# Kernel tuning notes

Measured on AMD Instinct MI355X. Metric: run time of the kernel, lower is better.

Reference implementation:

```python
import jax, jax.numpy as jnp
import numpy as np

B, K, V, D, T = 8, 4, 32000, 1024, 16
EOS, PAD = 2, 0
EOS_SCORE = 1000.0
BIG = 1e9  # suppresses beams 1..K-1 at step 0 (original starts from a single beam)


def setup_inputs() -> dict:
    key = jax.random.key(0)
    k1, k2, k3, k4 = jax.random.split(key, 4)
    s = 1.0 / np.sqrt(D)
    return {
        "words": jnp.ones((B, K), dtype=jnp.int32),  # BOS=1 on every beam
        "h0": jnp.zeros((B, K, D), dtype=jnp.float32),
        "c0": jnp.zeros((B, K, D), dtype=jnp.float32),
        "E": jax.random.normal(k1, (V, D), dtype=jnp.float32) * s,
        "Wx": jax.random.normal(k2, (D, 4 * D), dtype=jnp.float32) * s,
        "Wh": jax.random.normal(k3, (D, 4 * D), dtype=jnp.float32) * s,
        "b": jnp.zeros((4 * D,), dtype=jnp.float32),
        "Wout": jax.random.normal(k4, (D, V), dtype=jnp.float32) * s,
        "bout": jnp.zeros((V,), dtype=jnp.float32),
    }


def reference(words, h0, c0, E, Wx, Wh, b, Wout, bout):
    bidx = jnp.arange(B)[:, None]
    kidx = jnp.arange(K)[None, :]
    scores0 = jnp.concatenate(
        [jnp.zeros((B, 1), jnp.float32), jnp.full((B, K - 1), BIG, jnp.float32)], axis=1)
    buf0 = jnp.zeros((B, K, T), dtype=jnp.int32)
    stopped0 = jnp.zeros((B,), dtype=bool)

    def step(carry, j):
        w, scores, h, c, stopped, buf = carry
        # proc_word: embed -> LSTM cell -> vocab logits (vectorized over B*K beams)
        x = E[w]                                              # [B,K,D]
        gates = jnp.einsum('bkd,df->bkf', x, Wx) + jnp.einsum('bkd,df->bkf', h, Wh) + b
        i_, f_, g_, o_ = jnp.split(gates, 4, axis=-1)
        c_new = jax.nn.sigmoid(f_) * c + jax.nn.sigmoid(i_) * jnp.tanh(g_)
        h_new = jax.nn.sigmoid(o_) * jnp.tanh(c_new)
        logits = jnp.einsum('bkd,dv->bkv', h_new, Wout) + bout  # [B,K,V]
        p = -jax.nn.log_softmax(logits, axis=-1)                # negative log-probs
        neg_ps, idxs = jax.lax.top_k(-p, K)                     # K smallest per beam
        cand = (-neg_ps) + scores[:, :, None]                   # [B,K,K]
        flat = cand.reshape(B, K * K)
        wflat = idxs.reshape(B, K * K)
        neg_sel, sel = jax.lax.top_k(-flat, K)                  # K smallest over all cands
        sel_scores = -neg_sel                                   # [B,K]
        prev = sel // K                                         # originating beam
        new_w = jnp.take_along_axis(wflat, sel, axis=1)
        eos = new_w == EOS
        first_eos = eos[:, 0] & (~stopped)                      # best cand is EOS -> stop
        pen = eos & (~first_eos[:, None]) & (~stopped[:, None]) # non-best EOS penalized
        sel_scores = jnp.where(pen, EOS_SCORE, sel_scores)
        tok = jnp.where(first_eos[:, None], EOS, new_w)
        tok = jnp.where(stopped[:, None], PAD, tok)
        prevb = jnp.where(stopped[:, None], kidx, prev)         # stopped rows keep order
        buf = buf[bidx, prevb]                                  # reorder beam histories
        buf = buf.at[:, :, j].set(tok.astype(jnp.int32))
        h_new = h_new[bidx, prev]                               # gather per-beam states
        c_new = c_new[bidx, prev]
        scores = jnp.where(stopped[:, None], scores, sel_scores)
        w = jnp.where(stopped[:, None], w, new_w.astype(w.dtype))
        stopped = stopped | first_eos
        return (w, scores, h_new, c_new, stopped, buf), None

    carry0 = (words, scores0, h0, c0, stopped0, buf0)
    (_, scores, _, _, _, buf), _ = jax.lax.scan(step, carry0, jnp.arange(T))
    return buf, scores
```

## Files before the change

### kernel.cpp

```cpp
#include <hip/hip_runtime.h>
#include <math.h>
#include <float.h>

namespace {

constexpr int Bb = 8, Kk = 4, BKn = 32, Dd = 1024, Ff = 4096, Vv = 32000, Tt = 16;
constexpr int GDS = 32, GDC = 32;
constexpr int LTW = 64;
constexpr int LNB = Vv / LTW;
constexpr int LQC = 16;
constexpr int LQN = 16;
constexpr int NVCH = LNB;
constexpr int EOSt = 2, PADt = 0;
constexpr float BIGf = 1e9f, EOSSf = 1000.0f;

constexpr size_t OFF_HTN = 0;
constexpr size_t OFF_CB0 = OFF_HTN + (size_t)Dd * BKn;
constexpr size_t OFF_CB1 = OFF_CB0 + (size_t)BKn * Dd;
constexpr size_t OFF_GP  = OFF_CB1 + (size_t)BKn * Dd;
constexpr size_t OFF_CS  = OFF_GP  + (size_t)GDS * BKn * Ff;
constexpr size_t OFF_SC  = OFF_CS  + (size_t)NVCH * BKn * 12;
constexpr size_t OFF_INT = OFF_SC  + BKn;
constexpr int IW = 0, ISTOP = 32, IPREV = 40, IBUFA = 72, IBUFB = IBUFA + Bb * Kk * Tt;

__device__ __forceinline__ void cp16(const float* g, float* l) {
  __builtin_amdgcn_global_load_lds(
      (const __attribute__((address_space(1))) void*)g,
      (__attribute__((address_space(3))) void*)l, 16, 0, 0);
}

__device__ inline void ins4(float v, int id, float tv[4], int ti[4]) {
#pragma unroll
  for (int r = 0; r < 4; r++) {
    bool better = (v > tv[r]) || (v == tv[r] && id < ti[r]);
    if (better) { float fv = tv[r]; int fi = ti[r]; tv[r] = v; ti[r] = id; v = fv; id = fi; }
  }
}

template <int STARTOFF>
__device__ inline void merge_top4(float tv[4], int ti[4], float ov[4], int oi[4]) {
#pragma unroll
  for (int r = 0; r < 4; r++) {
    float hv = tv[0]; int hi = ti[0];
    float m = hv;
    for (int off = STARTOFF; off; off >>= 1) m = fmaxf(m, __shfl_xor(m, off));
    int c = (hv == m) ? hi : 0x7fffffff;
    for (int off = STARTOFF; off; off >>= 1) c = min(c, __shfl_xor(c, off));
    if (hv == m && hi == c) {
      tv[0] = tv[1]; ti[0] = ti[1];
      tv[1] = tv[2]; ti[1] = ti[2];
      tv[2] = tv[3]; ti[2] = ti[3];
      tv[3] = -FLT_MAX; ti[3] = 0x7fffffff;
    }
    ov[r] = m; oi[r] = c;
  }
}

__global__ __launch_bounds__(256) void initK(const int* __restrict__ words,
    const float* __restrict__ h0, const float* __restrict__ c0,
    float* __restrict__ ws) {
  int* wsi = (int*)(ws + OFF_INT);
  if (blockIdx.x < 128) {
    int g = blockIdx.x * 256 + threadIdx.x;
    int d = g >> 5, bk = g & 31;
    ws[OFF_HTN + g] = h0[(size_t)bk * Dd + d];
    ws[OFF_CB0 + g] = c0[g];
  } else {
    int t = threadIdx.x;
    if (t < BKn) {
      ws[OFF_SC + t] = ((t & 3) == 0) ? 0.f : BIGf;
      wsi[IW + t] = words[t];
      wsi[IPREV + t] = t & 3;
    }
    if (t < Bb) wsi[ISTOP + t] = 0;
    for (int i = t; i < 2 * Bb * Kk * Tt; i += 256) wsi[IBUFA + i] = 0;
  }
}

__global__ __launch_bounds__(256) void gatesK(const float* __restrict__ Wx,
    const float* __restrict__ Wh, const float* __restrict__ E,
    const float* __restrict__ hTn, const int* __restrict__ wsi,
    float* __restrict__ Gp) {
  __shared__ float xs[GDC][BKn], hs[GDC][BKn];
  int tid = threadIdx.x;
  int d0 = blockIdx.y * GDC;
  {
    int bk = tid & 31, dq = tid >> 5;
    int w = wsi[IW + bk];
    int src = (bk & ~3) | wsi[IPREV + bk];
    const float* Erow = E + (size_t)w * Dd + d0;
#pragma unroll
    for (int k = 0; k < 4; k++) {
      int d = dq * 4 + k;
      xs[d][bk] = Erow[d];
      hs[d][bk] = hTn[(size_t)(d0 + d) * BKn + src];
    }
  }
  __syncthreads();
  int ct = tid & 31, bg = tid >> 5;
  int f0 = blockIdx.x * 128 + ct * 4;
  float acc[4][4];
#pragma unroll
  for (int c = 0; c < 4; c++)
#pragma unroll
    for (int i = 0; i < 4; i++) acc[c][i] = 0.f;
#pragma unroll 4
  for (int d = 0; d < GDC; ++d) {
    float4 wx = *(const float4*)(Wx + (size_t)(d0 + d) * Ff + f0);
    float4 wh = *(const float4*)(Wh + (size_t)(d0 + d) * Ff + f0);
    float4 x4 = *(const float4*)&xs[d][bg * 4];
    float4 h4 = *(const float4*)&hs[d][bg * 4];
    float xv[4] = {x4.x, x4.y, x4.z, x4.w};
    float hv[4] = {h4.x, h4.y, h4.z, h4.w};
    float wxc[4] = {wx.x, wx.y, wx.z, wx.w};
    float whc[4] = {wh.x, wh.y, wh.z, wh.w};
#pragma unroll
    for (int c = 0; c < 4; c++)
#pragma unroll
      for (int i = 0; i < 4; i++)
        acc[c][i] = fmaf(xv[i], wxc[c], fmaf(hv[i], whc[c], acc[c][i]));
  }
#pragma unroll
  for (int i = 0; i < 4; i++) {
    int bk = bg * 4 + i;
    float4 o = {acc[0][i], acc[1][i], acc[2][i], acc[3][i]};
    *(float4*)(Gp + ((size_t)blockIdx.y * BKn + bk) * Ff + f0) = o;
  }
}

__global__ __launch_bounds__(256) void lstmK(const float* __restrict__ bvec,
    const float* __restrict__ Gp, const float* __restrict__ cPrev,
    const int* __restrict__ wsi, float* __restrict__ cNew,
    float* __restrict__ hTn) {
  __shared__ float part[4][128];
  int bk = blockIdx.x;
  int dcl = threadIdx.x & 127;
  int half = threadIdx.x >> 7;
  int dc = blockIdx.y * 128 + dcl;
  float s[4] = {0.f, 0.f, 0.f, 0.f};
#pragma unroll 4
  for (int dsl = 0; dsl < 16; dsl++) {
    int ds = half * 16 + dsl;
    const float* row = Gp + ((size_t)ds * BKn + bk) * Ff;
#pragma unroll
    for (int g = 0; g < 4; g++) s[g] += row[(size_t)g * Dd + dc];
  }
  if (half == 1) {
#pragma unroll
    for (int g = 0; g < 4; g++) part[g][dcl] = s[g];
  }
  __syncthreads();
  if (half == 0) {
    float gi = s[0] + part[0][dcl] + bvec[dc];
    float gf = s[1] + part[1][dcl] + bvec[Dd + dc];
    float gg = s[2] + part[2][dcl] + bvec[2 * Dd + dc];
    float go = s[3] + part[3][dcl] + bvec[3 * Dd + dc];
    int src = (bk & ~3) | wsi[IPREV + bk];
    float c = cPrev[(size_t)src * Dd + dc];
    float si = 1.f / (1.f + expf(-gi));
    float sf = 1.f / (1.f + expf(-gf));
    float so = 1.f / (1.f + expf(-go));
    float tg = tanhf(gg);
    float cn = sf * c + si * tg;
    float hn = so * tanhf(cn);
    cNew[(size_t)bk * Dd + dc] = cn;
    hTn[(size_t)dc * BKn + bk] = hn;
  }
}

__global__ __launch_bounds__(256) void logitsAK(const float* __restrict__ Wo,
    const float* __restrict__ bo, const float* __restrict__ hTn,
    float* __restrict__ cs) {
  __shared__ float wb[4][3][LQC][LTW];
  __shared__ float hb[4][3][LQC][BKn];
  __shared__ float sd[BKn][LTW];
  int tid = threadIdx.x;
  int q = tid >> 6;
  int lane = tid & 63;
  int cg = lane & 15;
  int bg = lane >> 4;
  size_t v0 = (size_t)blockIdx.x * LTW;
  int dq0 = q * 256;
  float acc[4][8];
#pragma unroll
  for (int c = 0; c < 4; c++)
#pragma unroll
    for (int i = 0; i < 8; i++) acc[c][i] = 0.f;

  float4 b4 = *(const float4*)(bo + v0 + cg * 4);

#define STAGE(CH, B)                                                          \
  {                                                                           \
    int d0_ = dq0 + (CH) * LQC;                                               \
    _Pragma("unroll") for (int i_ = 0; i_ < 4; i_++)                          \
      cp16(Wo + (size_t)(d0_ + i_ * 4 + (lane >> 4)) * Vv + v0 +              \
               (lane & 15) * 4,                                               \
           &wb[q][B][i_ * 4][0]);                                             \
    _Pragma("unroll") for (int j_ = 0; j_ < 2; j_++)                          \
      cp16(hTn + (size_t)(d0_ + j_ * 8 + (lane >> 3)) * BKn + (lane & 7) * 4, \
           &hb[q][B][j_ * 8][0]);                                             \
  }

  STAGE(0, 0)
  STAGE(1, 1)
  for (int k = 0; k < LQN; k++) {
    int b = k % 3;
    if (k + 2 < LQN) {
      STAGE(k + 2, (k + 2) % 3)
      asm volatile("s_waitcnt vmcnt(12)" ::: "memory");
    } else if (k + 1 < LQN) {
      asm volatile("s_waitcnt vmcnt(6)" ::: "memory");
    } else {
      asm volatile("s_waitcnt vmcnt(0)" ::: "memory");
    }
    __builtin_amdgcn_sched_barrier(0);
#pragma unroll 4
    for (int d = 0; d < LQC; d++) {
      float4 w4  = *(const float4*)&wb[q][b][d][cg * 4];
      float4 hlo = *(const float4*)&hb[q][b][d][bg * 8];
      float4 hhi = *(const float4*)&hb[q][b][d][bg * 8 + 4];
      float wv[4] = {w4.x, w4.y, w4.z, w4.w};
      float hv[8] = {hlo.x, hlo.y, hlo.z, hlo.w, hhi.x, hhi.y, hhi.z, hhi.w};
#pragma unroll
      for (int c = 0; c < 4; c++)
#pragma unroll
        for (int i = 0; i < 8; i++)
          acc[c][i] = fmaf(wv[c], hv[i], acc[c][i]);
    }
  }
#undef STAGE

  float bb[4] = {b4.x, b4.y, b4.z, b4.w};
  if (q == 0) {
#pragma unroll
    for (int c = 0; c < 4; c++)
#pragma unroll
      for (int i = 0; i < 8; i++)
        sd[bg * 8 + i][cg * 4 + c] = acc[c][i] + bb[c];
  }
  __syncthreads();
#pragma unroll
  for (int qq = 1; qq < 4; qq++) {
    if (q == qq) {
#pragma unroll
      for (int c = 0; c < 4; c++)
#pragma unroll
        for (int i = 0; i < 8; i++)
          sd[bg * 8 + i][cg * 4 + c] += acc[c][i];
    }
    __syncthreads();
  }

  int i0 = (int)v0 + lane;
  for (int bb_ = 0; bb_ < 8; ++bb_) {
    int bk = q * 8 + bb_;
    float v0f = sd[bk][lane];
    float m = v0f;
    for (int off = 32; off; off >>= 1) m = fmaxf(m, __shfl_xor(m, off));
    float se = expf(v0f - m);
    for (int off = 32; off; off >>= 1) se += __shfl_xor(se, off);
    float tv[4]; int ti[4];
#pragma unroll
    for (int r = 0; r < 4; r++) { tv[r] = -FLT_MAX; ti[r] = 0x7fffffff; }
    ins4(v0f, i0, tv, ti);
    float ov[4]; int oi[4];
    merge_top4<32>(tv, ti, ov, oi);
    if (lane == 0) {
      float* p = cs + ((size_t)blockIdx.x * BKn + bk) * 12;
      p[0] = m; p[1] = se;
#pragma unroll
      for (int r = 0; r < 4; r++) { p[2 + r] = ov[r]; p[6 + r] = __int_as_float(oi[r]); }
    }
  }
}

__global__ __launch_bounds__(1024) void redSelK(float* __restrict__ ws, int step) {
  __shared__ float bt_s[BKn][8];
  __shared__ int s_tok[BKn], s_prevb[BKn];
  int* wsi = (int*)(ws + OFF_INT);
  const float* cs = ws + OFF_CS;
  int tid = threadIdx.x;
  int wv = tid >> 6, lane = tid & 63;
  {
    int half = lane >> 5, l32 = lane & 31;
    int bk = wv * 2 + half;
    float tv[4]; int ti[4];
#pragma unroll
    for (int r = 0; r < 4; r++) { tv[r] = -FLT_MAX; ti[r] = 0x7fffffff; }
    float M = -FLT_MAX, ls = 0.f;
    for (int g = 0; g < 4; g++) {
      float4 pa[4], pb[4], pc[4];
      bool vv[4];
#pragma unroll
      for (int j = 0; j < 4; j++) {
        int c = l32 + 32 * (g * 4 + j);
        vv[j] = c < NVCH;
        const float* p = cs + ((size_t)c * BKn + bk) * 12;
        if (vv[j]) {
          pa[j] = *(const float4*)p;
          pb[j] = *(const float4*)(p + 4);
          pc[j] = *(const float4*)(p + 8);
        }
      }
#pragma unroll
      for (int j = 0; j < 4; j++) {
        if (vv[j]) {
          float cm = pa[j].x, csum = pa[j].y;
          if (cm > M) { ls *= expf(M - cm); M = cm; }
          ls += csum * expf(cm - M);
          ins4(pa[j].z, __float_as_int(pb[j].z), tv, ti);
          ins4(pa[j].w, __float_as_int(pb[j].w), tv, ti);
          ins4(pb[j].x, __float_as_int(pc[j].x), tv, ti);
          ins4(pb[j].y, __float_as_int(pc[j].y), tv, ti);
        }
      }
    }
    for (int off = 16; off; off >>= 1) {
      float Mo = __shfl_xor(M, off), lso = __shfl_xor(ls, off);
      float Mn = fmaxf(M, Mo);
      ls = ls * expf(M - Mn) + lso * expf(Mo - Mn);
      M = Mn;
    }
    float lse = M + logf(ls);
    float ov[4]; int oi[4];
    merge_top4<16>(tv, ti, ov, oi);
    if (l32 == 0) {
#pragma unroll
      for (int r = 0; r < 4; r++) {
        bt_s[bk][r] = lse - ov[r];
        bt_s[bk][4 + r] = __int_as_float(oi[r]);
      }
    }
  }
  __syncthreads();
  if (tid < Bb) {
    int b = tid;
    int st = wsi[ISTOP + b];
    float sc[4];
#pragma unroll
    for (int k = 0; k < 4; k++) sc[k] = ws[OFF_SC + b * 4 + k];
    float cval[16]; int ctok[16];
#pragma unroll
    for (int kb = 0; kb < 4; kb++)
#pragma unroll
      for (int r = 0; r < 4; r++) {
        cval[kb * 4 + r] = bt_s[b * 4 + kb][r] + sc[kb];
        ctok[kb * 4 + r] = __float_as_int(bt_s[b * 4 + kb][4 + r]);
      }
    float selS[4]; int selW[4], prevK[4];
    int usedMask = 0;
#pragma unroll
    for (int r = 0; r < 4; r++) {
      int best = -1; float bv = FLT_MAX;
#pragma unroll
      for (int t = 0; t < 16; t++) {
        if (!((usedMask >> t) & 1) && cval[t] < bv) { bv = cval[t]; best = t; }
      }
      usedMask |= 1 << best;
      int tok = 0;
#pragma unroll
      for (int t = 0; t < 16; t++) if (t == best) tok = ctok[t];
      selS[r] = bv; selW[r] = tok; prevK[r] = best >> 2;
    }
    bool eos[4];
#pragma unroll
    for (int r = 0; r < 4; r++) eos[r] = (selW[r] == EOSt);
    bool first = eos[0] && !st;
#pragma unroll
    for (int r = 0; r < 4; r++) if (eos[r] && !first && !st) selS[r] = EOSSf;
#pragma unroll
    for (int k = 0; k < 4; k++) {
      int tok = st ? PADt : (first ? EOSt : selW[k]);
      int pb  = st ? k : prevK[k];
      s_tok[b * 4 + k] = tok;
      s_prevb[b * 4 + k] = pb;
      if (!st) { ws[OFF_SC + b * 4 + k] = selS[k]; wsi[IW + b * 4 + k] = selW[k]; }
      wsi[IPREV + b * 4 + k] = prevK[k];
    }
    wsi[ISTOP + b] = (st || first) ? 1 : 0;
  }
  __syncthreads();
  if (tid < 512) {
    const int* br = wsi + (((step & 1) == 0) ? IBUFA : IBUFB);
    int* bw = wsi + (((step & 1) == 0) ? IBUFB : IBUFA);
    int bkk = tid >> 4, t = tid & 15;
    int pb = s_prevb[bkk];
    int src = ((bkk & ~3) | pb) * Tt + t;
    int val = br[src];
    if (t == step) val = s_tok[bkk];
    bw[tid] = val;
  }
}

__global__ __launch_bounds__(256) void outK(const float* __restrict__ ws,
                                            float* __restrict__ out) {
  const int* wsi = (const int*)(ws + OFF_INT);
  int g = blockIdx.x * 256 + threadIdx.x;
  if (g < Bb * Kk * Tt) {
    out[g] = (float)wsi[IBUFA + g];
  } else if (g < Bb * Kk * Tt + BKn) {
    out[g] = ws[OFF_SC + (g - Bb * Kk * Tt)];
  }
}

}

extern "C" void kernel_launch(void* const* d_in, const int* in_sizes, int n_in,
                              void* d_out, int out_size, void* d_ws, size_t ws_size,
                              hipStream_t stream) {
  (void)in_sizes; (void)n_in; (void)out_size; (void)ws_size;
  const int*   words = (const int*)d_in[0];
  const float* h0 = (const float*)d_in[1];
  const float* c0 = (const float*)d_in[2];
  const float* E  = (const float*)d_in[3];
  const float* Wx = (const float*)d_in[4];
  const float* Wh = (const float*)d_in[5];
  const float* bv = (const float*)d_in[6];
  const float* Wo = (const float*)d_in[7];
  const float* bo = (const float*)d_in[8];
  float* ws = (float*)d_ws;
  float* hTn = ws + OFF_HTN;
  float* cb0 = ws + OFF_CB0;
  float* cb1 = ws + OFF_CB1;
  float* Gp  = ws + OFF_GP;
  float* cs  = ws + OFF_CS;
  int*   wsi = (int*)(ws + OFF_INT);

  initK<<<129, 256, 0, stream>>>(words, h0, c0, ws);
  for (int j = 0; j < Tt; j++) {
    float* cPrev = (j & 1) ? cb1 : cb0;
    float* cNext = (j & 1) ? cb0 : cb1;
    gatesK<<<dim3(32, GDS), 256, 0, stream>>>(Wx, Wh, E, hTn, wsi, Gp);
    lstmK<<<dim3(32, 8), 256, 0, stream>>>(bv, Gp, cPrev, wsi, cNext, hTn);
    logitsAK<<<LNB, 256, 0, stream>>>(Wo, bo, hTn, cs);
    redSelK<<<1, 1024, 0, stream>>>(ws, j);
  }
  outK<<<3, 256, 0, stream>>>(ws, (float*)d_out);
}
```

Baseline: 1.729 ms.

## Restructure gates GEMV with async LDS staging and in-block split-K reduction

The gates kernel now gives each block a 128-wide slice of D and 64 gate columns, where the old kernel used 32-wide D slices. Wx/Wh tiles are staged through a triple-buffered shared-memory pipeline using async 16-byte copies with explicit vmcnt waits. Four wavefronts each handle a quarter of the D slice and reduce their partials in shared memory before a coalesced store. This cuts the number of D-split partial sums written to global memory from 32 to 8, so the LSTM kernel reads fewer partials. In exchange it adds serialized shared-memory reduction passes and heavier LDS use per block.

```diff
diff --git a/kernel.cpp b/kernel.cpp
--- a/kernel.cpp
+++ b/kernel.cpp
@@ -5,7 +5,7 @@
 namespace {
 
 constexpr int Bb = 8, Kk = 4, BKn = 32, Dd = 1024, Ff = 4096, Vv = 32000, Tt = 16;
-constexpr int GDS = 32, GDC = 32;
+constexpr int GDS = 8;
 constexpr int LTW = 64;
 constexpr int LNB = Vv / LTW;
 constexpr int LQC = 16;
@@ -77,54 +77,110 @@
   }
 }
 
-__global__ __launch_bounds__(256) void gatesK(const float* __restrict__ Wx,
+__global__ __launch_bounds__(256) void gatesAK(const float* __restrict__ Wx,
     const float* __restrict__ Wh, const float* __restrict__ E,
     const float* __restrict__ hTn, const int* __restrict__ wsi,
     float* __restrict__ Gp) {
-  __shared__ float xs[GDC][BKn], hs[GDC][BKn];
+  __shared__ float wxb[4][3][4][64];
+  __shared__ float whb[4][3][4][64];
+  __shared__ float xs[128][BKn];
+  __shared__ float hs[128][BKn];
+  __shared__ float sd[BKn][64];
   int tid = threadIdx.x;
-  int d0 = blockIdx.y * GDC;
+  int q = tid >> 6;
+  int lane = tid & 63;
+  int cg = lane & 15;
+  int bg = lane >> 4;
+  int f0 = blockIdx.x * 64;
+  int dblk0 = blockIdx.y * 128;
+
   {
     int bk = tid & 31, dq = tid >> 5;
     int w = wsi[IW + bk];
     int src = (bk & ~3) | wsi[IPREV + bk];
-    const float* Erow = E + (size_t)w * Dd + d0;
-#pragma unroll
-    for (int k = 0; k < 4; k++) {
-      int d = dq * 4 + k;
+    const float* Erow = E + (size_t)w * Dd + dblk0;
+#pragma unroll
+    for (int k = 0; k < 16; k++) {
+      int d = dq * 16 + k;
       xs[d][bk] = Erow[d];
-      hs[d][bk] = hTn[(size_t)(d0 + d) * BKn + src];
-    }
-  }
-  __syncthreads();
-  int ct = tid & 31, bg = tid >> 5;
-  int f0 = blockIdx.x * 128 + ct * 4;
-  float acc[4][4];
+      hs[d][bk] = hTn[(size_t)(dblk0 + d) * BKn + src];
+    }
+  }
+  __syncthreads();
+
+  float acc[4][8];
 #pragma unroll
   for (int c = 0; c < 4; c++)
 #pragma unroll
-    for (int i = 0; i < 4; i++) acc[c][i] = 0.f;
-#pragma unroll 4
-  for (int d = 0; d < GDC; ++d) {
-    float4 wx = *(const float4*)(Wx + (size_t)(d0 + d) * Ff + f0);
-    float4 wh = *(const float4*)(Wh + (size_t)(d0 + d) * Ff + f0);
-    float4 x4 = *(const float4*)&xs[d][bg * 4];
-    float4 h4 = *(const float4*)&hs[d][bg * 4];
-    float xv[4] = {x4.x, x4.y, x4.z, x4.w};
-    float hv[4] = {h4.x, h4.y, h4.z, h4.w};
-    float wxc[4] = {wx.x, wx.y, wx.z, wx.w};
-    float whc[4] = {wh.x, wh.y, wh.z, wh.w};
+    for (int i = 0; i < 8; i++) acc[c][i] = 0.f;
+
+#define STAGE(CH, B)                                                          \
+  {                                                                           \
+    int gd_ = dblk0 + q * 32 + (CH) * 4 + (lane >> 4);                        \
+    cp16(Wx + (size_t)gd_ * Ff + f0 + (lane & 15) * 4, &wxb[q][B][0][0]);     \
+    cp16(Wh + (size_t)gd_ * Ff + f0 + (lane & 15) * 4, &whb[q][B][0][0]);     \
+  }
+
+  STAGE(0, 0)
+  STAGE(1, 1)
+  for (int k = 0; k < 8; k++) {
+    int b = k % 3;
+    if (k + 2 < 8) {
+      STAGE(k + 2, (k + 2) % 3)
+      asm volatile("s_waitcnt vmcnt(4)" ::: "memory");
+    } else if (k + 1 < 8) {
+      asm volatile("s_waitcnt vmcnt(2)" ::: "memory");
+    } else {
+      asm volatile("s_waitcnt vmcnt(0)" ::: "memory");
+    }
+    __builtin_amdgcn_sched_barrier(0);
+    int ldb = q * 32 + k * 4;
+#pragma unroll
+    for (int d = 0; d < 4; d++) {
+      float4 wx4 = *(const float4*)&wxb[q][b][d][cg * 4];
+      float4 wh4 = *(const float4*)&whb[q][b][d][cg * 4];
+      float4 xlo = *(const float4*)&xs[ldb + d][bg * 8];
+      float4 xhi = *(const float4*)&xs[ldb + d][bg * 8 + 4];
+      float4 hlo = *(const float4*)&hs[ldb + d][bg * 8];
+      float4 hhi = *(const float4*)&hs[ldb + d][bg * 8 + 4];
+      float wxc[4] = {wx4.x, wx4.y, wx4.z, wx4.w};
+      float whc[4] = {wh4.x, wh4.y, wh4.z, wh4.w};
+      float xv[8] = {xlo.x, xlo.y, xlo.z, xlo.w, xhi.x, xhi.y, xhi.z, xhi.w};
+      float hv[8] = {hlo.x, hlo.y, hlo.z, hlo.w, hhi.x, hhi.y, hhi.z, hhi.w};
+#pragma unroll
+      for (int c = 0; c < 4; c++)
+#pragma unroll
+        for (int i = 0; i < 8; i++)
+          acc[c][i] = fmaf(xv[i], wxc[c], fmaf(hv[i], whc[c], acc[c][i]));
+    }
+  }
+#undef STAGE
+
+  if (q == 0) {
 #pragma unroll
     for (int c = 0; c < 4; c++)
 #pragma unroll
-      for (int i = 0; i < 4; i++)
-        acc[c][i] = fmaf(xv[i], wxc[c], fmaf(hv[i], whc[c], acc[c][i]));
-  }
-#pragma unroll
-  for (int i = 0; i < 4; i++) {
-    int bk = bg * 4 + i;
-    float4 o = {acc[0][i], acc[1][i], acc[2][i], acc[3][i]};
-    *(float4*)(Gp + ((size_t)blockIdx.y * BKn + bk) * Ff + f0) = o;
+      for (int i = 0; i < 8; i++)
+        sd[bg * 8 + i][cg * 4 + c] = acc[c][i];
+  }
+  __syncthreads();
+#pragma unroll
+  for (int qq = 1; qq < 4; qq++) {
+    if (q == qq) {
+#pragma unroll
+      for (int c = 0; c < 4; c++)
+#pragma unroll
+        for (int i = 0; i < 8; i++)
+          sd[bg * 8 + i][cg * 4 + c] += acc[c][i];
+    }
+    __syncthreads();
+  }
+
+  {
+    int row = tid >> 3, c8 = tid & 7;
+    float* dst = Gp + ((size_t)blockIdx.y * BKn + row) * Ff + f0 + c8 * 8;
+    *(float4*)dst       = *(const float4*)&sd[row][c8 * 8];
+    *(float4*)(dst + 4) = *(const float4*)&sd[row][c8 * 8 + 4];
   }
 }
 
@@ -138,9 +194,9 @@
   int half = threadIdx.x >> 7;
   int dc = blockIdx.y * 128 + dcl;
   float s[4] = {0.f, 0.f, 0.f, 0.f};
-#pragma unroll 4
-  for (int dsl = 0; dsl < 16; dsl++) {
-    int ds = half * 16 + dsl;
+#pragma unroll
+  for (int dsl = 0; dsl < 4; dsl++) {
+    int ds = half * 4 + dsl;
     const float* row = Gp + ((size_t)ds * BKn + bk) * Ff;
 #pragma unroll
     for (int g = 0; g < 4; g++) s[g] += row[(size_t)g * Dd + dc];
@@ -430,7 +486,7 @@
   for (int j = 0; j < Tt; j++) {
     float* cPrev = (j & 1) ? cb1 : cb0;
     float* cNext = (j & 1) ? cb0 : cb1;
-    gatesK<<<dim3(32, GDS), 256, 0, stream>>>(Wx, Wh, E, hTn, wsi, Gp);
+    gatesAK<<<dim3(64, GDS), 256, 0, stream>>>(Wx, Wh, E, hTn, wsi, Gp);
     lstmK<<<dim3(32, 8), 256, 0, stream>>>(bv, Gp, cPrev, wsi, cNext, hTn);
     logitsAK<<<LNB, 256, 0, stream>>>(Wo, bo, hTn, cs);
     redSelK<<<1, 1024, 0, stream>>>(ws, j);
```

Result: faster. 1.664 ms (median of 2 runs) (-3.7%).
